# Kernel optimization log

Hardware: AMD Instinct MI355X
Metric: run time of the kernel (lower is better)

The kernel has to match this reference:

```python
import jax, jax.numpy as jnp
import numpy as np

N = 50000       # nodes
E_RAND = 800000 # random edges (avg degree 16); self loops appended
IN, HID, H, OUT = 256, 64, 4, 256
NEG_SLOPE = 0.2


def setup_inputs() -> dict:
    key = jax.random.key(0)
    ks = jax.random.split(key, 8)
    x = jax.random.normal(ks[0], (N, IN), dtype=jnp.float32)
    er = jax.random.randint(ks[1], (2, E_RAND), 0, N, dtype=jnp.int32)
    loops = jnp.arange(N, dtype=jnp.int32)
    edge_index = jnp.concatenate([er, jnp.stack([loops, loops])], axis=1)  # [2, E_RAND+N]
    # xavier-ish scaled params
    W1 = jax.random.normal(ks[2], (H * HID, IN), jnp.float32) * (2.0 / (IN + H * HID)) ** 0.5
    a1_src = jax.random.normal(ks[3], (H, HID), jnp.float32) * 0.1
    a1_dst = jax.random.normal(ks[4], (H, HID), jnp.float32) * 0.1
    W2 = jax.random.normal(ks[5], (OUT, H * HID), jnp.float32) * (2.0 / (H * HID + OUT)) ** 0.5
    a2_src = jax.random.normal(ks[6], (1, OUT), jnp.float32) * 0.1
    a2_dst = jax.random.normal(ks[7], (1, OUT), jnp.float32) * 0.1
    return {"x": x, "edge_index": edge_index, "W1": W1, "a1_src": a1_src,
            "a1_dst": a1_dst, "W2": W2, "a2_src": a2_src, "a2_dst": a2_dst}


def gat_layer(h, W, a_src, a_dst, src, dst, concat):
    n = h.shape[0]
    nh, nf = a_src.shape
    hp = (h @ W.T).reshape(n, nh, nf)                 # [N,H,F]
    e = (hp[src] * a_src).sum(-1) + (hp[dst] * a_dst).sum(-1)  # [E,H]
    e = jnp.where(e > 0, e, NEG_SLOPE * e)            # leaky_relu
    e_max = jax.ops.segment_max(e, dst, num_segments=n)
    ex = jnp.exp(e - e_max[dst])
    e_sum = jax.ops.segment_sum(ex, dst, num_segments=n)
    alpha = ex / (e_sum[dst] + 1e-16)                 # [E,H]
    out = jax.ops.segment_sum(hp[src] * alpha[..., None], dst, num_segments=n)
    return out.reshape(n, nh * nf) if concat else out.mean(axis=1)


def reference(x, edge_index, W1, a1_src, a1_dst, W2, a2_src, a2_dst):
    src, dst = edge_index[0], edge_index[1]
    h = jax.nn.relu(gat_layer(x, W1, a1_src, a1_dst, src, dst, True))
    return gat_layer(h, W2, a2_src, a2_dst, src, dst, False)
```

## Files before the change

kernel.cpp:

```cpp
#include <hip/hip_runtime.h>
#include <math.h>


typedef __attribute__((ext_vector_type(8))) short short8;
typedef __attribute__((ext_vector_type(4))) float f32x4;
typedef _Float16 half8 __attribute__((ext_vector_type(8)));

__device__ inline short f2bf(float f) {
    unsigned u = __float_as_uint(f);
    unsigned r = (u + 0x7FFF + ((u >> 16) & 1)) >> 16;
    return (short)r;
}
__device__ inline float bf2f(short b) {
    return __uint_as_float(((unsigned)(unsigned short)b) << 16);
}
__device__ inline unsigned short f2h(float f) {
    _Float16 h = (_Float16)f;
    unsigned short u;
    __builtin_memcpy(&u, &h, 2);
    return u;
}
__device__ inline float h2f(unsigned short u) {
    _Float16 h;
    __builtin_memcpy(&h, &u, 2);
    return (float)h;
}

__global__ void convert_w(const float* __restrict__ W, short* __restrict__ Whi,
                          short* __restrict__ Wlo, int n) {
    int i = blockIdx.x * 256 + threadIdx.x;
    if (i < n) {
        float v = W[i];
        short h = f2bf(v);
        Whi[i] = h;
        Wlo[i] = f2bf(v - bf2f(h));
    }
}

__global__ __launch_bounds__(256) void gemm_mfma(const float* __restrict__ A,
                                                 const short* __restrict__ Bh_g,
                                                 const short* __restrict__ Bl_g,
                                                 unsigned short* __restrict__ C, int M) {
    __shared__ short Ah[128 * 40];
    __shared__ short Al[128 * 40];
    __shared__ short Bh[128 * 40];
    __shared__ short Bl[128 * 40];
    const int tid = threadIdx.x;
    const int m0 = blockIdx.x * 128;
    const int n0 = blockIdx.y * 128;
    const int w = tid >> 6, lane = tid & 63;
    const int l15 = lane & 15, q = lane >> 4;

    f32x4 acc[2][8];
    #pragma unroll
    for (int mt = 0; mt < 2; ++mt)
        #pragma unroll
        for (int nt = 0; nt < 8; ++nt) acc[mt][nt] = (f32x4){0.f, 0.f, 0.f, 0.f};

    const int ar = tid >> 1;
    const int ak = (tid & 1) * 16;

    for (int k0 = 0; k0 < 256; k0 += 32) {
        int gm = m0 + ar;
        float4 v0, v1, v2, v3;
        if (gm < M) {
            const float* ap = &A[(size_t)gm * 256 + k0 + ak];
            v0 = *(const float4*)(ap);
            v1 = *(const float4*)(ap + 4);
            v2 = *(const float4*)(ap + 8);
            v3 = *(const float4*)(ap + 12);
        } else {
            v0 = make_float4(0.f, 0.f, 0.f, 0.f);
            v1 = v0; v2 = v0; v3 = v0;
        }
        float av[16] = {v0.x, v0.y, v0.z, v0.w, v1.x, v1.y, v1.z, v1.w,
                        v2.x, v2.y, v2.z, v2.w, v3.x, v3.y, v3.z, v3.w};
        short8 hi0, hi1, lo0, lo1;
        #pragma unroll
        for (int j = 0; j < 8; ++j) {
            short h = f2bf(av[j]);
            hi0[j] = h;
            lo0[j] = f2bf(av[j] - bf2f(h));
        }
        #pragma unroll
        for (int j = 0; j < 8; ++j) {
            short h = f2bf(av[8 + j]);
            hi1[j] = h;
            lo1[j] = f2bf(av[8 + j] - bf2f(h));
        }
        *(short8*)&Ah[ar * 40 + ak]     = hi0;
        *(short8*)&Ah[ar * 40 + ak + 8] = hi1;
        *(short8*)&Al[ar * 40 + ak]     = lo0;
        *(short8*)&Al[ar * 40 + ak + 8] = lo1;
        {
            const short* s0 = &Bh_g[(size_t)(n0 + ar) * 256 + k0 + ak];
            *(short8*)&Bh[ar * 40 + ak]     = *(const short8*)s0;
            *(short8*)&Bh[ar * 40 + ak + 8] = *(const short8*)(s0 + 8);
            const short* s1 = &Bl_g[(size_t)(n0 + ar) * 256 + k0 + ak];
            *(short8*)&Bl[ar * 40 + ak]     = *(const short8*)s1;
            *(short8*)&Bl[ar * 40 + ak + 8] = *(const short8*)(s1 + 8);
        }
        __syncthreads();
        short8 ahi[2], alo[2];
        #pragma unroll
        for (int mt = 0; mt < 2; ++mt) {
            int rowA = w * 32 + mt * 16 + l15;
            ahi[mt] = *(short8*)&Ah[rowA * 40 + q * 8];
            alo[mt] = *(short8*)&Al[rowA * 40 + q * 8];
        }
        #pragma unroll
        for (int nt = 0; nt < 8; ++nt) {
            int rowB = nt * 16 + l15;
            short8 bhi = *(short8*)&Bh[rowB * 40 + q * 8];
            short8 blo = *(short8*)&Bl[rowB * 40 + q * 8];
            #pragma unroll
            for (int mt = 0; mt < 2; ++mt) {
                acc[mt][nt] = __builtin_amdgcn_mfma_f32_16x16x32_bf16(ahi[mt], bhi, acc[mt][nt], 0, 0, 0);
                acc[mt][nt] = __builtin_amdgcn_mfma_f32_16x16x32_bf16(alo[mt], bhi, acc[mt][nt], 0, 0, 0);
                acc[mt][nt] = __builtin_amdgcn_mfma_f32_16x16x32_bf16(ahi[mt], blo, acc[mt][nt], 0, 0, 0);
            }
        }
        __syncthreads();
    }
    #pragma unroll
    for (int mt = 0; mt < 2; ++mt) {
        #pragma unroll
        for (int nt = 0; nt < 8; ++nt) {
            #pragma unroll
            for (int r = 0; r < 4; ++r) {
                int gm = m0 + w * 32 + mt * 16 + q * 4 + r;
                if (gm < M) C[(size_t)gm * 256 + n0 + nt * 16 + l15] = f2h(acc[mt][nt][r]);
            }
        }
    }
}

__global__ void zero_int(int* __restrict__ p, int n) {
    int i = blockIdx.x * 256 + threadIdx.x;
    if (i < n) p[i] = 0;
}

__global__ void hist_kernel(const int* __restrict__ dst, int* __restrict__ deg, int E) {
    int i = blockIdx.x * 256 + threadIdx.x;
    if (i < E) atomicAdd(&deg[dst[i]], 1);
}

__global__ __launch_bounds__(1024) void scan1(const int* __restrict__ deg,
                                              int* __restrict__ lex,
                                              int* __restrict__ bsums, int n) {
    __shared__ int sh[1024];
    int tid = threadIdx.x;
    int i = blockIdx.x * 1024 + tid;
    int v = (i < n) ? deg[i] : 0;
    sh[tid] = v;
    __syncthreads();
    #pragma unroll
    for (int off = 1; off < 1024; off <<= 1) {
        int t2 = (tid >= off) ? sh[tid - off] : 0;
        __syncthreads();
        sh[tid] += t2;
        __syncthreads();
    }
    if (i < n) lex[i] = sh[tid] - v;
    if (tid == 1023) bsums[blockIdx.x] = sh[1023];
}

__global__ __launch_bounds__(1024) void scan2(const int* __restrict__ bsums,
                                              int* __restrict__ boffs,
                                              int* __restrict__ offs, int nb, int n) {
    __shared__ int sh[1024];
    int tid = threadIdx.x;
    int v = (tid < nb) ? bsums[tid] : 0;
    sh[tid] = v;
    __syncthreads();
    #pragma unroll
    for (int off = 1; off < 1024; off <<= 1) {
        int t2 = (tid >= off) ? sh[tid - off] : 0;
        __syncthreads();
        sh[tid] += t2;
        __syncthreads();
    }
    if (tid < nb) boffs[tid] = sh[tid] - v;
    if (tid == nb - 1) offs[n] = sh[tid];
}

__global__ __launch_bounds__(1024) void scan3(int* __restrict__ offs,
                                              int* __restrict__ cur,
                                              const int* __restrict__ boffs, int n) {
    int i = blockIdx.x * 1024 + threadIdx.x;
    if (i < n) {
        int o = offs[i] + boffs[blockIdx.x];
        offs[i] = o;
        cur[i] = o;
    }
}

__global__ void scatter_kernel(const int* __restrict__ src, const int* __restrict__ dst,
                               int* __restrict__ cur, int* __restrict__ sorted, int E) {
    int i = blockIdx.x * 256 + threadIdx.x;
    if (i < E) {
        int p = atomicAdd(&cur[dst[i]], 1);
        sorted[p] = src[i];
    }
}

template <int NH>
__global__ __launch_bounds__(256) void scompute(const unsigned short* __restrict__ hp,
                                                const float* __restrict__ a_src,
                                                const float* __restrict__ a_dst,
                                                float* __restrict__ s_src,
                                                float* __restrict__ s_dst, int N) {
    const int w = threadIdx.x >> 6, lane = threadIdx.x & 63;
    const int node = blockIdx.x * 4 + w;
    if (node >= N) return;
    const int f0 = lane * 4;
    ushort4 uv = *(const ushort4*)(hp + (size_t)node * 256 + f0);
    float4 as = *(const float4*)(a_src + f0);
    float4 ad = *(const float4*)(a_dst + f0);
    float x0 = h2f(uv.x), x1 = h2f(uv.y), x2 = h2f(uv.z), x3 = h2f(uv.w);
    float p1 = x0 * as.x + x1 * as.y + x2 * as.z + x3 * as.w;
    float p2 = x0 * ad.x + x1 * ad.y + x2 * ad.z + x3 * ad.w;
    if constexpr (NH == 4) {
        #pragma unroll
        for (int off = 1; off < 16; off <<= 1) {
            p1 += __shfl_xor(p1, off, 64);
            p2 += __shfl_xor(p2, off, 64);
        }
        if ((lane & 15) == 0) {
            s_src[node * 4 + (lane >> 4)] = p1;
            s_dst[node * 4 + (lane >> 4)] = p2;
        }
    } else {
        #pragma unroll
        for (int off = 1; off < 64; off <<= 1) {
            p1 += __shfl_xor(p1, off, 64);
            p2 += __shfl_xor(p2, off, 64);
        }
        if (lane == 0) {
            s_src[node] = p1;
            s_dst[node] = p2;
        }
    }
}

template <int NH, bool RELU>
__global__ __launch_bounds__(256) void aggregate4(const unsigned short* __restrict__ hp,
                                                  const float* __restrict__ ssrc,
                                                  const float* __restrict__ sdst,
                                                  const int* __restrict__ offs,
                                                  const int* __restrict__ sorted,
                                                  float* __restrict__ out, int N) {
    __shared__ int   s_sh[4][64];
    __shared__ float p_sh[4][64][NH];

    const int w = threadIdx.x >> 6, lane = threadIdx.x & 63;
    const int node_raw = blockIdx.x * 4 + w;
    const bool node_ok = node_raw < N;
    const int node = node_ok ? node_raw : (N - 1);
    constexpr int NF = 256 / NH;

    const int b = offs[node], e = offs[node + 1];
    const int deg = e - b;

    float sv[NH];
    #pragma unroll
    for (int h = 0; h < NH; ++h) sv[h] = sdst[node * NH + h];

    float lv[NH], mx[NH];
    const bool small = (deg <= 64);

    if (small) {
        int key = (lane < deg) ? sorted[b + lane] : 0x7FFFFFFF;
        #pragma unroll
        for (int k = 2; k <= 64; k <<= 1) {
            #pragma unroll
            for (int j = k >> 1; j > 0; j >>= 1) {
                int other = __shfl_xor(key, j, 64);
                bool keepMin = ((lane & j) == 0) == ((lane & k) == 0);
                int mn = min(key, other), mh = max(key, other);
                key = keepMin ? mn : mh;
            }
        }
        const bool valid = lane < deg;
        const int mys = valid ? key : 0;

        float evv[NH];
        if constexpr (NH == 4) {
            float4 sa = *(const float4*)&ssrc[(size_t)mys * 4];
            evv[0] = sa.x + sv[0]; evv[1] = sa.y + sv[1];
            evv[2] = sa.z + sv[2]; evv[3] = sa.w + sv[3];
        } else {
            evv[0] = ssrc[mys] + sv[0];
        }
        #pragma unroll
        for (int h = 0; h < NH; ++h) {
            float ev = evv[h];
            ev = ev > 0.f ? ev : 0.2f * ev;
            evv[h] = valid ? ev : -INFINITY;
            mx[h] = evv[h];
        }
        #pragma unroll
        for (int off = 32; off > 0; off >>= 1)
            #pragma unroll
            for (int h = 0; h < NH; ++h)
                mx[h] = fmaxf(mx[h], __shfl_xor(mx[h], off, 64));

        float pv[NH];
        #pragma unroll
        for (int h = 0; h < NH; ++h) {
            pv[h] = valid ? __expf(evv[h] - mx[h]) : 0.f;
            lv[h] = pv[h];
        }
        #pragma unroll
        for (int off = 32; off > 0; off >>= 1)
            #pragma unroll
            for (int h = 0; h < NH; ++h)
                lv[h] += __shfl_xor(lv[h], off, 64);

        s_sh[w][lane] = mys;
        #pragma unroll
        for (int h = 0; h < NH; ++h) p_sh[w][lane][h] = pv[h];
    } else {
        #pragma unroll
        for (int h = 0; h < NH; ++h) mx[h] = -INFINITY;
        for (int c = b + lane; c < e; c += 64) {
            int s = sorted[c];
            #pragma unroll
            for (int h = 0; h < NH; ++h) {
                float ev = ssrc[s * NH + h] + sv[h];
                ev = ev > 0.f ? ev : 0.2f * ev;
                mx[h] = fmaxf(mx[h], ev);
            }
        }
        #pragma unroll
        for (int off = 32; off > 0; off >>= 1)
            #pragma unroll
            for (int h = 0; h < NH; ++h)
                mx[h] = fmaxf(mx[h], __shfl_xor(mx[h], off, 64));
    }

    __syncthreads();

    if (small) {
        const int quarter = lane >> 4;
        const int l16 = lane & 15;
        const int f0 = l16 * 16;
        const int head = f0 / NF;

        float acc[16];
        #pragma unroll
        for (int k = 0; k < 16; ++k) acc[k] = 0.f;

        const int iters = (deg + 3) >> 2;
        for (int t2 = 0; t2 < iters; ++t2) {
            int j = 4 * t2 + quarter;
            bool jv = j < deg;
            int jj = jv ? j : 0;
            int s = s_sh[w][jj];
            float p = jv ? p_sh[w][jj][head] : 0.f;
            const unsigned short* row = hp + (size_t)s * 256 + f0;
            half8 v0 = *(const half8*)(row);
            half8 v1 = *(const half8*)(row + 8);
            #pragma unroll
            for (int k = 0; k < 8; ++k) {
                acc[k]     = fmaf(p, (float)v0[k], acc[k]);
                acc[8 + k] = fmaf(p, (float)v1[k], acc[8 + k]);
            }
        }
        #pragma unroll
        for (int k = 0; k < 16; ++k) {
            acc[k] += __shfl_xor(acc[k], 16, 64);
            acc[k] += __shfl_xor(acc[k], 32, 64);
        }
        if (node_ok && lane < 16) {
            float li = 1.0f / (lv[head] + 1e-16f);
            float o[16];
            #pragma unroll
            for (int k = 0; k < 16; ++k) {
                o[k] = acc[k] * li;
                if (RELU) o[k] = fmaxf(o[k], 0.f);
            }
            float* op = &out[(size_t)node * 256 + f0];
            *(float4*)&op[0]  = make_float4(o[0], o[1], o[2], o[3]);
            *(float4*)&op[4]  = make_float4(o[4], o[5], o[6], o[7]);
            *(float4*)&op[8]  = make_float4(o[8], o[9], o[10], o[11]);
            *(float4*)&op[12] = make_float4(o[12], o[13], o[14], o[15]);
        }
    } else {
        const int half = lane >> 5;
        const int l32 = lane & 31;
        const int f0 = l32 * 8;
        const int head = f0 / NF;

        float acc[8];
        #pragma unroll
        for (int k = 0; k < 8; ++k) acc[k] = 0.f;
        #pragma unroll
        for (int h = 0; h < NH; ++h) lv[h] = 0.f;

        int last = -1, round = 0;
        for (;;) {
            int myMin = 0x7FFFFFFF, myCnt = 0;
            for (int c = b + lane; c < e; c += 64) {
                int s = sorted[c];
                if (s > last) {
                    if (s < myMin) { myMin = s; myCnt = 1; }
                    else if (s == myMin) ++myCnt;
                }
            }
            #pragma unroll
            for (int off = 32; off > 0; off >>= 1) {
                int om = __shfl_xor(myMin, off, 64);
                int oc = __shfl_xor(myCnt, off, 64);
                if (om < myMin) { myMin = om; myCnt = oc; }
                else if (om == myMin) myCnt += oc;
            }
            if (myMin == 0x7FFFFFFF) break;
            const bool mine = ((round & 1) == half);
            float cf = (float)myCnt;
            float ph[NH];
            #pragma unroll
            for (int h = 0; h < NH; ++h) {
                float ev = ssrc[myMin * NH + h] + sv[h];
                ev = ev > 0.f ? ev : 0.2f * ev;
                ph[h] = __expf(ev - mx[h]);
            }
            if (mine && l32 == 0) {
                #pragma unroll
                for (int h = 0; h < NH; ++h) lv[h] += cf * ph[h];
            }
            if (mine) {
                float p = cf * ph[head];
                half8 v = *(const half8*)(hp + (size_t)myMin * 256 + f0);
                #pragma unroll
                for (int k = 0; k < 8; ++k) acc[k] = fmaf(p, (float)v[k], acc[k]);
            }
            last = myMin; ++round;
        }
        #pragma unroll
        for (int off = 32; off > 0; off >>= 1)
            #pragma unroll
            for (int h = 0; h < NH; ++h)
                lv[h] += __shfl_xor(lv[h], off, 64);

        #pragma unroll
        for (int k = 0; k < 8; ++k) acc[k] += __shfl_xor(acc[k], 32, 64);

        if (node_ok && lane < 32) {
            float li = 1.0f / (lv[head] + 1e-16f);
            float o[8];
            #pragma unroll
            for (int k = 0; k < 8; ++k) {
                o[k] = acc[k] * li;
                if (RELU) o[k] = fmaxf(o[k], 0.f);
            }
            *(float4*)&out[(size_t)node * 256 + f0]     = make_float4(o[0], o[1], o[2], o[3]);
            *(float4*)&out[(size_t)node * 256 + f0 + 4] = make_float4(o[4], o[5], o[6], o[7]);
        }
    }
}

extern "C" void kernel_launch(void* const* d_in, const int* in_sizes, int n_in,
                              void* d_out, int out_size, void* d_ws, size_t ws_size,
                              hipStream_t stream) {
    const float* x   = (const float*)d_in[0];
    const int*   ei  = (const int*)d_in[1];
    const float* W1  = (const float*)d_in[2];
    const float* a1s = (const float*)d_in[3];
    const float* a1d = (const float*)d_in[4];
    const float* W2  = (const float*)d_in[5];
    const float* a2s = (const float*)d_in[6];
    const float* a2d = (const float*)d_in[7];
    float* out = (float*)d_out;

    const int N = in_sizes[0] / 256;
    const int E = in_sizes[1] / 2;
    const int* src = ei;
    const int* dst = ei + E;

    unsigned short* hp = (unsigned short*)d_ws;
    float* ssrc  = (float*)(hp + (size_t)N * 256);
    float* sdst  = ssrc + (size_t)N * 4;
    int*   deg   = (int*)(sdst + (size_t)N * 4);
    int*   cur   = deg + N;
    int*   offs  = cur + N;
    int*   sorted= offs + N + 1;
    int*   bsums = sorted + E;
    int*   boffs = bsums + 64;
    short* w1hi  = (short*)(boffs + 64);
    short* w1lo  = w1hi + 65536;
    short* w2hi  = w1lo + 65536;
    short* w2lo  = w2hi + 65536;

    const int nb = (N + 1023) / 1024;

    convert_w<<<256, 256, 0, stream>>>(W1, w1hi, w1lo, 65536);
    convert_w<<<256, 256, 0, stream>>>(W2, w2hi, w2lo, 65536);

    zero_int<<<(N + 255) / 256, 256, 0, stream>>>(deg, N);
    hist_kernel<<<(E + 255) / 256, 256, 0, stream>>>(dst, deg, E);
    scan1<<<nb, 1024, 0, stream>>>(deg, offs, bsums, N);
    scan2<<<1, 1024, 0, stream>>>(bsums, boffs, offs, nb, N);
    scan3<<<nb, 1024, 0, stream>>>(offs, cur, boffs, N);
    scatter_kernel<<<(E + 255) / 256, 256, 0, stream>>>(src, dst, cur, sorted, E);

    dim3 gg((N + 127) / 128, 2);
    int aggblocks = (N + 3) / 4;

    gemm_mfma<<<gg, 256, 0, stream>>>(x, w1hi, w1lo, hp, N);
    scompute<4><<<aggblocks, 256, 0, stream>>>(hp, a1s, a1d, ssrc, sdst, N);
    aggregate4<4, true><<<aggblocks, 256, 0, stream>>>(hp, ssrc, sdst, offs, sorted, out, N);

    gemm_mfma<<<gg, 256, 0, stream>>>(out, w2hi, w2lo, hp, N);
    scompute<1><<<aggblocks, 256, 0, stream>>>(hp, a2s, a2d, ssrc, sdst, N);
    aggregate4<1, false><<<aggblocks, 256, 0, stream>>>(hp, ssrc, sdst, offs, sorted, out, N);
}
```

Before: 428.1 us.

## Pre-split GEMM inputs to bf16 hi/lo, hoist CSR sort, prefetch aggregate rows

A new convert_x8 kernel splits x into bf16 hi/lo halves once, stored in the output buffer. The layer-1 aggregation now writes its activations directly as bf16 hi/lo, so both GEMMs load pre-split shorts instead of converting fp32 on every tile. The per-node bitonic sort of neighbour lists moves out of both aggregate calls into a single sort_csr pass. The aggregate loop also software-prefetches the next neighbour index and weight. The aim is to cut redundant conversion ALU work and one duplicated sort, at the cost of an extra kernel and extra memory traffic for the x conversion.

New measurement: 454.0 us. +6.1%, slower.

```diff
diff --git a/kernel.cpp b/kernel.cpp
--- a/kernel.cpp
+++ b/kernel.cpp
@@ -37,7 +37,34 @@
     }
 }
 
-__global__ __launch_bounds__(256) void gemm_mfma(const float* __restrict__ A,
+__global__ void convert_x8(const float* __restrict__ X, short* __restrict__ Xhi,
+                           short* __restrict__ Xlo, long n) {
+    long i = ((long)blockIdx.x * 256 + threadIdx.x) * 8;
+    if (i + 8 <= n) {
+        float4 v0 = *(const float4*)&X[i];
+        float4 v1 = *(const float4*)&X[i + 4];
+        float av[8] = {v0.x, v0.y, v0.z, v0.w, v1.x, v1.y, v1.z, v1.w};
+        short8 hi, lo;
+        #pragma unroll
+        for (int j = 0; j < 8; ++j) {
+            short h = f2bf(av[j]);
+            hi[j] = h;
+            lo[j] = f2bf(av[j] - bf2f(h));
+        }
+        *(short8*)&Xhi[i] = hi;
+        *(short8*)&Xlo[i] = lo;
+    } else {
+        for (long k = i; k < n; ++k) {
+            float v = X[k];
+            short h = f2bf(v);
+            Xhi[k] = h;
+            Xlo[k] = f2bf(v - bf2f(h));
+        }
+    }
+}
+
+__global__ __launch_bounds__(256) void gemm_mfma(const short* __restrict__ Ah_g,
+                                                 const short* __restrict__ Al_g,
                                                  const short* __restrict__ Bh_g,
                                                  const short* __restrict__ Bl_g,
                                                  unsigned short* __restrict__ C, int M) {
@@ -62,36 +89,20 @@
 
     for (int k0 = 0; k0 < 256; k0 += 32) {
         int gm = m0 + ar;
-        float4 v0, v1, v2, v3;
         if (gm < M) {
-            const float* ap = &A[(size_t)gm * 256 + k0 + ak];
-            v0 = *(const float4*)(ap);
-            v1 = *(const float4*)(ap + 4);
-            v2 = *(const float4*)(ap + 8);
-            v3 = *(const float4*)(ap + 12);
+            const short* a0 = &Ah_g[(size_t)gm * 256 + k0 + ak];
+            *(short8*)&Ah[ar * 40 + ak]     = *(const short8*)a0;
+            *(short8*)&Ah[ar * 40 + ak + 8] = *(const short8*)(a0 + 8);
+            const short* a1 = &Al_g[(size_t)gm * 256 + k0 + ak];
+            *(short8*)&Al[ar * 40 + ak]     = *(const short8*)a1;
+            *(short8*)&Al[ar * 40 + ak + 8] = *(const short8*)(a1 + 8);
         } else {
-            v0 = make_float4(0.f, 0.f, 0.f, 0.f);
-            v1 = v0; v2 = v0; v3 = v0;
-        }
-        float av[16] = {v0.x, v0.y, v0.z, v0.w, v1.x, v1.y, v1.z, v1.w,
-                        v2.x, v2.y, v2.z, v2.w, v3.x, v3.y, v3.z, v3.w};
-        short8 hi0, hi1, lo0, lo1;
-        #pragma unroll
-        for (int j = 0; j < 8; ++j) {
-            short h = f2bf(av[j]);
-            hi0[j] = h;
-            lo0[j] = f2bf(av[j] - bf2f(h));
-        }
-        #pragma unroll
-        for (int j = 0; j < 8; ++j) {
-            short h = f2bf(av[8 + j]);
-            hi1[j] = h;
-            lo1[j] = f2bf(av[8 + j] - bf2f(h));
-        }
-        *(short8*)&Ah[ar * 40 + ak]     = hi0;
-        *(short8*)&Ah[ar * 40 + ak + 8] = hi1;
-        *(short8*)&Al[ar * 40 + ak]     = lo0;
-        *(short8*)&Al[ar * 40 + ak + 8] = lo1;
+            short8 z = (short8){0, 0, 0, 0, 0, 0, 0, 0};
+            *(short8*)&Ah[ar * 40 + ak]     = z;
+            *(short8*)&Ah[ar * 40 + ak + 8] = z;
+            *(short8*)&Al[ar * 40 + ak]     = z;
+            *(short8*)&Al[ar * 40 + ak + 8] = z;
+        }
         {
             const short* s0 = &Bh_g[(size_t)(n0 + ar) * 256 + k0 + ak];
             *(short8*)&Bh[ar * 40 + ak]     = *(const short8*)s0;
@@ -202,6 +213,28 @@
         int p = atomicAdd(&cur[dst[i]], 1);
         sorted[p] = src[i];
     }
+}
+
+__global__ __launch_bounds__(256) void sort_csr(const int* __restrict__ offs,
+                                                int* __restrict__ sorted, int N) {
+    const int w = threadIdx.x >> 6, lane = threadIdx.x & 63;
+    const int node = blockIdx.x * 4 + w;
+    if (node >= N) return;
+    const int b = offs[node], e = offs[node + 1];
+    const int deg = e - b;
+    if (deg < 2 || deg > 64) return;
+    int key = (lane < deg) ? sorted[b + lane] : 0x7FFFFFFF;
+    #pragma unroll
+    for (int k = 2; k <= 64; k <<= 1) {
+        #pragma unroll
+        for (int j = k >> 1; j > 0; j >>= 1) {
+            int other = __shfl_xor(key, j, 64);
+            bool keepMin = ((lane & j) == 0) == ((lane & k) == 0);
+            int mn = min(key, other), mh = max(key, other);
+            key = keepMin ? mn : mh;
+        }
+    }
+    if (lane < deg) sorted[b + lane] = key;
 }
 
 template <int NH>
@@ -243,13 +276,15 @@
     }
 }
 
-template <int NH, bool RELU>
+template <int NH, bool RELU, bool SPLIT>
 __global__ __launch_bounds__(256) void aggregate4(const unsigned short* __restrict__ hp,
                                                   const float* __restrict__ ssrc,
                                                   const float* __restrict__ sdst,
                                                   const int* __restrict__ offs,
                                                   const int* __restrict__ sorted,
-                                                  float* __restrict__ out, int N) {
+                                                  float* __restrict__ out,
+                                                  short* __restrict__ ohi,
+                                                  short* __restrict__ olo, int N) {
     __shared__ int   s_sh[4][64];
     __shared__ float p_sh[4][64][NH];
 
@@ -270,19 +305,8 @@
     const bool small = (deg <= 64);
 
     if (small) {
-        int key = (lane < deg) ? sorted[b + lane] : 0x7FFFFFFF;
-        #pragma unroll
-        for (int k = 2; k <= 64; k <<= 1) {
-            #pragma unroll
-            for (int j = k >> 1; j > 0; j >>= 1) {
-                int other = __shfl_xor(key, j, 64);
-                bool keepMin = ((lane & j) == 0) == ((lane & k) == 0);
-                int mn = min(key, other), mh = max(key, other);
-                key = keepMin ? mn : mh;
-            }
-        }
         const bool valid = lane < deg;
-        const int mys = valid ? key : 0;
+        const int mys = valid ? sorted[b + lane] : 0;
 
         float evv[NH];
         if constexpr (NH == 4) {
@@ -352,19 +376,25 @@
         for (int k = 0; k < 16; ++k) acc[k] = 0.f;
 
         const int iters = (deg + 3) >> 2;
+        int j = quarter;
+        bool jv = j < deg;
+        int jj = jv ? j : 0;
+        int s = s_sh[w][jj];
+        float p = jv ? p_sh[w][jj][head] : 0.f;
         for (int t2 = 0; t2 < iters; ++t2) {
-            int j = 4 * t2 + quarter;
-            bool jv = j < deg;
-            int jj = jv ? j : 0;
-            int s = s_sh[w][jj];
-            float p = jv ? p_sh[w][jj][head] : 0.f;
             const unsigned short* row = hp + (size_t)s * 256 + f0;
             half8 v0 = *(const half8*)(row);
             half8 v1 = *(const half8*)(row + 8);
+            float pc = p;
+            int jn = 4 * (t2 + 1) + quarter;
+            bool jvn = jn < deg;
+            int jjn = jvn ? jn : 0;
+            s = s_sh[w][jjn];
+            p = jvn ? p_sh[w][jjn][head] : 0.f;
             #pragma unroll
             for (int k = 0; k < 8; ++k) {
-                acc[k]     = fmaf(p, (float)v0[k], acc[k]);
-                acc[8 + k] = fmaf(p, (float)v1[k], acc[8 + k]);
+                acc[k]     = fmaf(pc, (float)v0[k], acc[k]);
+                acc[8 + k] = fmaf(pc, (float)v1[k], acc[8 + k]);
             }
         }
         #pragma unroll
@@ -380,11 +410,26 @@
                 o[k] = acc[k] * li;
                 if (RELU) o[k] = fmaxf(o[k], 0.f);
             }
-            float* op = &out[(size_t)node * 256 + f0];
-            *(float4*)&op[0]  = make_float4(o[0], o[1], o[2], o[3]);
-            *(float4*)&op[4]  = make_float4(o[4], o[5], o[6], o[7]);
-            *(float4*)&op[8]  = make_float4(o[8], o[9], o[10], o[11]);
-            *(float4*)&op[12] = make_float4(o[12], o[13], o[14], o[15]);
+            if constexpr (SPLIT) {
+                short8 h0, h1, l0, l1;
+                #pragma unroll
+                for (int k = 0; k < 8; ++k) {
+                    short hh = f2bf(o[k]);
+                    h0[k] = hh; l0[k] = f2bf(o[k] - bf2f(hh));
+                    short hh2 = f2bf(o[8 + k]);
+                    h1[k] = hh2; l1[k] = f2bf(o[8 + k] - bf2f(hh2));
+                }
+                *(short8*)&ohi[(size_t)node * 256 + f0]     = h0;
+                *(short8*)&ohi[(size_t)node * 256 + f0 + 8] = h1;
+                *(short8*)&olo[(size_t)node * 256 + f0]     = l0;
+                *(short8*)&olo[(size_t)node * 256 + f0 + 8] = l1;
+            } else {
+                float* op = &out[(size_t)node * 256 + f0];
+                *(float4*)&op[0]  = make_float4(o[0], o[1], o[2], o[3]);
+                *(float4*)&op[4]  = make_float4(o[4], o[5], o[6], o[7]);
+                *(float4*)&op[8]  = make_float4(o[8], o[9], o[10], o[11]);
+                *(float4*)&op[12] = make_float4(o[12], o[13], o[14], o[15]);
+            }
         }
     } else {
         const int half = lane >> 5;
@@ -454,8 +499,19 @@
                 o[k] = acc[k] * li;
                 if (RELU) o[k] = fmaxf(o[k], 0.f);
             }
-            *(float4*)&out[(size_t)node * 256 + f0]     = make_float4(o[0], o[1], o[2], o[3]);
-            *(float4*)&out[(size_t)node * 256 + f0 + 4] = make_float4(o[4], o[5], o[6], o[7]);
+            if constexpr (SPLIT) {
+                short8 h0, l0;
+                #pragma unroll
+                for (int k = 0; k < 8; ++k) {
+                    short hh = f2bf(o[k]);
+                    h0[k] = hh; l0[k] = f2bf(o[k] - bf2f(hh));
+                }
+                *(short8*)&ohi[(size_t)node * 256 + f0] = h0;
+                *(short8*)&olo[(size_t)node * 256 + f0] = l0;
+            } else {
+                *(float4*)&out[(size_t)node * 256 + f0]     = make_float4(o[0], o[1], o[2], o[3]);
+                *(float4*)&out[(size_t)node * 256 + f0 + 4] = make_float4(o[4], o[5], o[6], o[7]);
+            }
         }
     }
 }
@@ -492,10 +548,15 @@
     short* w2hi  = w1lo + 65536;
     short* w2lo  = w2hi + 65536;
 
+    short* xhi = (short*)d_out;
+    short* xlo = xhi + (size_t)N * 256;
+
     const int nb = (N + 1023) / 1024;
 
     convert_w<<<256, 256, 0, stream>>>(W1, w1hi, w1lo, 65536);
     convert_w<<<256, 256, 0, stream>>>(W2, w2hi, w2lo, 65536);
+    long nx = (long)N * 256;
+    convert_x8<<<(int)((nx / 8 + 255) / 256), 256, 0, stream>>>(x, xhi, xlo, nx);
 
     zero_int<<<(N + 255) / 256, 256, 0, stream>>>(deg, N);
     hist_kernel<<<(E + 255) / 256, 256, 0, stream>>>(dst, deg, E);
@@ -506,12 +567,15 @@
 
     dim3 gg((N + 127) / 128, 2);
     int aggblocks = (N + 3) / 4;
-
-    gemm_mfma<<<gg, 256, 0, stream>>>(x, w1hi, w1lo, hp, N);
+    sort_csr<<<aggblocks, 256, 0, stream>>>(offs, sorted, N);
+
+    gemm_mfma<<<gg, 256, 0, stream>>>(xhi, xlo, w1hi, w1lo, hp, N);
     scompute<4><<<aggblocks, 256, 0, stream>>>(hp, a1s, a1d, ssrc, sdst, N);
-    aggregate4<4, true><<<aggblocks, 256, 0, stream>>>(hp, ssrc, sdst, offs, sorted, out, N);
-
-    gemm_mfma<<<gg, 256, 0, stream>>>(out, w2hi, w2lo, hp, N);
+    aggregate4<4, true, true><<<aggblocks, 256, 0, stream>>>(hp, ssrc, sdst, offs, sorted,
+                                                             nullptr, xhi, xlo, N);
+
+    gemm_mfma<<<gg, 256, 0, stream>>>(xhi, xlo, w2hi, w2lo, hp, N);
     scompute<1><<<aggblocks, 256, 0, stream>>>(hp, a2s, a2d, ssrc, sdst, N);
-    aggregate4<1, false><<<aggblocks, 256, 0, stream>>>(hp, ssrc, sdst, offs, sorted, out, N);
-}
+    aggregate4<1, false, false><<<aggblocks, 256, 0, stream>>>(hp, ssrc, sdst, offs, sorted,
+                                                               out, nullptr, nullptr, N);
+}
```

## Switch GEMMs to single-pass fp16 MFMA and hoist per-node neighbor sort

Applied to the files above, without the earlier changes.

Replaces the three-pass split-bf16 GEMM (hi/lo emulation of fp32) with a single fp16 MFMA pass. Inputs x and the layer-1 activations are now stored as fp16, the latter written straight from aggregate4, with d_out reused as scratch. The bitonic sort of each node's neighbor list moves out of both aggregate passes into one sort_csr kernel that runs once. This cuts MFMA work and the bytes the GEMMs read, but lowers GEMM input precision to fp16 and adds a conversion pass over x.

Result: faster. 414.6 us (-3.2%).

```diff
diff --git a/kernel.cpp b/kernel.cpp
--- a/kernel.cpp
+++ b/kernel.cpp
@@ -3,17 +3,10 @@
 
 
 typedef __attribute__((ext_vector_type(8))) short short8;
+typedef __attribute__((ext_vector_type(8))) unsigned short ushort8;
 typedef __attribute__((ext_vector_type(4))) float f32x4;
 typedef _Float16 half8 __attribute__((ext_vector_type(8)));
 
-__device__ inline short f2bf(float f) {
-    unsigned u = __float_as_uint(f);
-    unsigned r = (u + 0x7FFF + ((u >> 16) & 1)) >> 16;
-    return (short)r;
-}
-__device__ inline float bf2f(short b) {
-    return __uint_as_float(((unsigned)(unsigned short)b) << 16);
-}
 __device__ inline unsigned short f2h(float f) {
     _Float16 h = (_Float16)f;
     unsigned short u;
@@ -26,25 +19,26 @@
     return (float)h;
 }
 
-__global__ void convert_w(const float* __restrict__ W, short* __restrict__ Whi,
-                          short* __restrict__ Wlo, int n) {
-    int i = blockIdx.x * 256 + threadIdx.x;
-    if (i < n) {
-        float v = W[i];
-        short h = f2bf(v);
-        Whi[i] = h;
-        Wlo[i] = f2bf(v - bf2f(h));
-    }
-}
-
-__global__ __launch_bounds__(256) void gemm_mfma(const float* __restrict__ A,
-                                                 const short* __restrict__ Bh_g,
-                                                 const short* __restrict__ Bl_g,
+__global__ void convert_h8(const float* __restrict__ X, unsigned short* __restrict__ Xh,
+                           long n) {
+    long i = ((long)blockIdx.x * 256 + threadIdx.x) * 8;
+    if (i + 8 <= n) {
+        float4 v0 = *(const float4*)&X[i];
+        float4 v1 = *(const float4*)&X[i + 4];
+        ushort8 o;
+        o[0] = f2h(v0.x); o[1] = f2h(v0.y); o[2] = f2h(v0.z); o[3] = f2h(v0.w);
+        o[4] = f2h(v1.x); o[5] = f2h(v1.y); o[6] = f2h(v1.z); o[7] = f2h(v1.w);
+        *(ushort8*)&Xh[i] = o;
+    } else {
+        for (long k = i; k < n; ++k) Xh[k] = f2h(X[k]);
+    }
+}
+
+__global__ __launch_bounds__(256) void gemm_mfma(const unsigned short* __restrict__ A_g,
+                                                 const unsigned short* __restrict__ B_g,
                                                  unsigned short* __restrict__ C, int M) {
-    __shared__ short Ah[128 * 40];
-    __shared__ short Al[128 * 40];
-    __shared__ short Bh[128 * 40];
-    __shared__ short Bl[128 * 40];
+    __shared__ unsigned short Ah[128 * 40];
+    __shared__ unsigned short Bh[128 * 40];
     const int tid = threadIdx.x;
     const int m0 = blockIdx.x * 128;
     const int n0 = blockIdx.y * 128;
@@ -62,63 +56,34 @@
 
     for (int k0 = 0; k0 < 256; k0 += 32) {
         int gm = m0 + ar;
-        float4 v0, v1, v2, v3;
         if (gm < M) {
-            const float* ap = &A[(size_t)gm * 256 + k0 + ak];
-            v0 = *(const float4*)(ap);
-            v1 = *(const float4*)(ap + 4);
-            v2 = *(const float4*)(ap + 8);
-            v3 = *(const float4*)(ap + 12);
+            const unsigned short* a0 = &A_g[(size_t)gm * 256 + k0 + ak];
+            *(ushort8*)&Ah[ar * 40 + ak]     = *(const ushort8*)a0;
+            *(ushort8*)&Ah[ar * 40 + ak + 8] = *(const ushort8*)(a0 + 8);
         } else {
-            v0 = make_float4(0.f, 0.f, 0.f, 0.f);
-            v1 = v0; v2 = v0; v3 = v0;
-        }
-        float av[16] = {v0.x, v0.y, v0.z, v0.w, v1.x, v1.y, v1.z, v1.w,
-                        v2.x, v2.y, v2.z, v2.w, v3.x, v3.y, v3.z, v3.w};
-        short8 hi0, hi1, lo0, lo1;
-        #pragma unroll
-        for (int j = 0; j < 8; ++j) {
-            short h = f2bf(av[j]);
-            hi0[j] = h;
-            lo0[j] = f2bf(av[j] - bf2f(h));
-        }
-        #pragma unroll
-        for (int j = 0; j < 8; ++j) {
-            short h = f2bf(av[8 + j]);
-            hi1[j] = h;
-            lo1[j] = f2bf(av[8 + j] - bf2f(h));
-        }
-        *(short8*)&Ah[ar * 40 + ak]     = hi0;
-        *(short8*)&Ah[ar * 40 + ak + 8] = hi1;
-        *(short8*)&Al[ar * 40 + ak]     = lo0;
-        *(short8*)&Al[ar * 40 + ak + 8] = lo1;
+            ushort8 z = (ushort8){0, 0, 0, 0, 0, 0, 0, 0};
+            *(ushort8*)&Ah[ar * 40 + ak]     = z;
+            *(ushort8*)&Ah[ar * 40 + ak + 8] = z;
+        }
         {
-            const short* s0 = &Bh_g[(size_t)(n0 + ar) * 256 + k0 + ak];
-            *(short8*)&Bh[ar * 40 + ak]     = *(const short8*)s0;
-            *(short8*)&Bh[ar * 40 + ak + 8] = *(const short8*)(s0 + 8);
-            const short* s1 = &Bl_g[(size_t)(n0 + ar) * 256 + k0 + ak];
-            *(short8*)&Bl[ar * 40 + ak]     = *(const short8*)s1;
-            *(short8*)&Bl[ar * 40 + ak + 8] = *(const short8*)(s1 + 8);
+            const unsigned short* b0 = &B_g[(size_t)(n0 + ar) * 256 + k0 + ak];
+            *(ushort8*)&Bh[ar * 40 + ak]     = *(const ushort8*)b0;
+            *(ushort8*)&Bh[ar * 40 + ak + 8] = *(const ushort8*)(b0 + 8);
         }
         __syncthreads();
-        short8 ahi[2], alo[2];
+        half8 a[2];
         #pragma unroll
         for (int mt = 0; mt < 2; ++mt) {
             int rowA = w * 32 + mt * 16 + l15;
-            ahi[mt] = *(short8*)&Ah[rowA * 40 + q * 8];
-            alo[mt] = *(short8*)&Al[rowA * 40 + q * 8];
+            a[mt] = *(half8*)&Ah[rowA * 40 + q * 8];
         }
         #pragma unroll
         for (int nt = 0; nt < 8; ++nt) {
             int rowB = nt * 16 + l15;
-            short8 bhi = *(short8*)&Bh[rowB * 40 + q * 8];
-            short8 blo = *(short8*)&Bl[rowB * 40 + q * 8];
-            #pragma unroll
-            for (int mt = 0; mt < 2; ++mt) {
-                acc[mt][nt] = __builtin_amdgcn_mfma_f32_16x16x32_bf16(ahi[mt], bhi, acc[mt][nt], 0, 0, 0);
-                acc[mt][nt] = __builtin_amdgcn_mfma_f32_16x16x32_bf16(alo[mt], bhi, acc[mt][nt], 0, 0, 0);
-                acc[mt][nt] = __builtin_amdgcn_mfma_f32_16x16x32_bf16(ahi[mt], blo, acc[mt][nt], 0, 0, 0);
-            }
+            half8 bf = *(half8*)&Bh[rowB * 40 + q * 8];
+            #pragma unroll
+            for (int mt = 0; mt < 2; ++mt)
+                acc[mt][nt] = __builtin_amdgcn_mfma_f32_16x16x32_f16(a[mt], bf, acc[mt][nt], 0, 0, 0);
         }
         __syncthreads();
     }
@@ -202,6 +167,28 @@
         int p = atomicAdd(&cur[dst[i]], 1);
         sorted[p] = src[i];
     }
+}
+
+__global__ __launch_bounds__(256) void sort_csr(const int* __restrict__ offs,
+                                                int* __restrict__ sorted, int N) {
+    const int w = threadIdx.x >> 6, lane = threadIdx.x & 63;
+    const int node = blockIdx.x * 4 + w;
+    if (node >= N) return;
+    const int b = offs[node], e = offs[node + 1];
+    const int deg = e - b;
+    if (deg < 2 || deg > 64) return;
+    int key = (lane < deg) ? sorted[b + lane] : 0x7FFFFFFF;
+    #pragma unroll
+    for (int k = 2; k <= 64; k <<= 1) {
+        #pragma unroll
+        for (int j = k >> 1; j > 0; j >>= 1) {
+            int other = __shfl_xor(key, j, 64);
+            bool keepMin = ((lane & j) == 0) == ((lane & k) == 0);
+            int mn = min(key, other), mh = max(key, other);
+            key = keepMin ? mn : mh;
+        }
+    }
+    if (lane < deg) sorted[b + lane] = key;
 }
 
 template <int NH>
@@ -243,13 +230,14 @@
     }
 }
 
-template <int NH, bool RELU>
+template <int NH, bool RELU, bool F16OUT>
 __global__ __launch_bounds__(256) void aggregate4(const unsigned short* __restrict__ hp,
                                                   const float* __restrict__ ssrc,
                                                   const float* __restrict__ sdst,
                                                   const int* __restrict__ offs,
                                                   const int* __restrict__ sorted,
-                                                  float* __restrict__ out, int N) {
+                                                  float* __restrict__ out,
+                                                  unsigned short* __restrict__ outh, int N) {
     __shared__ int   s_sh[4][64];
     __shared__ float p_sh[4][64][NH];
 
@@ -270,19 +258,8 @@
     const bool small = (deg <= 64);
 
     if (small) {
-        int key = (lane < deg) ? sorted[b + lane] : 0x7FFFFFFF;
-        #pragma unroll
-        for (int k = 2; k <= 64; k <<= 1) {
-            #pragma unroll
-            for (int j = k >> 1; j > 0; j >>= 1) {
-                int other = __shfl_xor(key, j, 64);
-                bool keepMin = ((lane & j) == 0) == ((lane & k) == 0);
-                int mn = min(key, other), mh = max(key, other);
-                key = keepMin ? mn : mh;
-            }
-        }
         const bool valid = lane < deg;
-        const int mys = valid ? key : 0;
+        const int mys = valid ? sorted[b + lane] : 0;
 
         float evv[NH];
         if constexpr (NH == 4) {
@@ -380,11 +357,22 @@
                 o[k] = acc[k] * li;
                 if (RELU) o[k] = fmaxf(o[k], 0.f);
             }
-            float* op = &out[(size_t)node * 256 + f0];
-            *(float4*)&op[0]  = make_float4(o[0], o[1], o[2], o[3]);
-            *(float4*)&op[4]  = make_float4(o[4], o[5], o[6], o[7]);
-            *(float4*)&op[8]  = make_float4(o[8], o[9], o[10], o[11]);
-            *(float4*)&op[12] = make_float4(o[12], o[13], o[14], o[15]);
+            if constexpr (F16OUT) {
+                ushort8 u0, u1;
+                #pragma unroll
+                for (int k = 0; k < 8; ++k) {
+                    u0[k] = f2h(o[k]);
+                    u1[k] = f2h(o[8 + k]);
+                }
+                *(ushort8*)&outh[(size_t)node * 256 + f0]     = u0;
+                *(ushort8*)&outh[(size_t)node * 256 + f0 + 8] = u1;
+            } else {
+                float* op = &out[(size_t)node * 256 + f0];
+                *(float4*)&op[0]  = make_float4(o[0], o[1], o[2], o[3]);
+                *(float4*)&op[4]  = make_float4(o[4], o[5], o[6], o[7]);
+                *(float4*)&op[8]  = make_float4(o[8], o[9], o[10], o[11]);
+                *(float4*)&op[12] = make_float4(o[12], o[13], o[14], o[15]);
+            }
         }
     } else {
         const int half = lane >> 5;
@@ -454,8 +442,15 @@
                 o[k] = acc[k] * li;
                 if (RELU) o[k] = fmaxf(o[k], 0.f);
             }
-            *(float4*)&out[(size_t)node * 256 + f0]     = make_float4(o[0], o[1], o[2], o[3]);
-            *(float4*)&out[(size_t)node * 256 + f0 + 4] = make_float4(o[4], o[5], o[6], o[7]);
+            if constexpr (F16OUT) {
+                ushort8 u0;
+                #pragma unroll
+                for (int k = 0; k < 8; ++k) u0[k] = f2h(o[k]);
+                *(ushort8*)&outh[(size_t)node * 256 + f0] = u0;
+            } else {
+                *(float4*)&out[(size_t)node * 256 + f0]     = make_float4(o[0], o[1], o[2], o[3]);
+                *(float4*)&out[(size_t)node * 256 + f0 + 4] = make_float4(o[4], o[5], o[6], o[7]);
+            }
         }
     }
 }
@@ -487,15 +482,18 @@
     int*   sorted= offs + N + 1;
     int*   bsums = sorted + E;
     int*   boffs = bsums + 64;
-    short* w1hi  = (short*)(boffs + 64);
-    short* w1lo  = w1hi + 65536;
-    short* w2hi  = w1lo + 65536;
-    short* w2lo  = w2hi + 65536;
+    unsigned short* w1h = (unsigned short*)(boffs + 64);
+    unsigned short* w2h = w1h + 65536;
+
+    unsigned short* xh = (unsigned short*)d_out;
+    unsigned short* hh = xh + (size_t)N * 256;
 
     const int nb = (N + 1023) / 1024;
 
-    convert_w<<<256, 256, 0, stream>>>(W1, w1hi, w1lo, 65536);
-    convert_w<<<256, 256, 0, stream>>>(W2, w2hi, w2lo, 65536);
+    convert_h8<<<32, 256, 0, stream>>>(W1, w1h, 65536);
+    convert_h8<<<32, 256, 0, stream>>>(W2, w2h, 65536);
+    long nx = (long)N * 256;
+    convert_h8<<<(int)((nx / 8 + 255) / 256), 256, 0, stream>>>(x, xh, nx);
 
     zero_int<<<(N + 255) / 256, 256, 0, stream>>>(deg, N);
     hist_kernel<<<(E + 255) / 256, 256, 0, stream>>>(dst, deg, E);
@@ -506,12 +504,15 @@
 
     dim3 gg((N + 127) / 128, 2);
     int aggblocks = (N + 3) / 4;
-
-    gemm_mfma<<<gg, 256, 0, stream>>>(x, w1hi, w1lo, hp, N);
+    sort_csr<<<aggblocks, 256, 0, stream>>>(offs, sorted, N);
+
+    gemm_mfma<<<gg, 256, 0, stream>>>(xh, w1h, hp, N);
     scompute<4><<<aggblocks, 256, 0, stream>>>(hp, a1s, a1d, ssrc, sdst, N);
-    aggregate4<4, true><<<aggblocks, 256, 0, stream>>>(hp, ssrc, sdst, offs, sorted, out, N);
-
-    gemm_mfma<<<gg, 256, 0, stream>>>(out, w2hi, w2lo, hp, N);
+    aggregate4<4, true, true><<<aggblocks, 256, 0, stream>>>(hp, ssrc, sdst, offs, sorted,
+                                                             nullptr, hh, N);
+
+    gemm_mfma<<<gg, 256, 0, stream>>>(hh, w2h, hp, N);
     scompute<1><<<aggblocks, 256, 0, stream>>>(hp, a2s, a2d, ssrc, sdst, N);
-    aggregate4<1, false><<<aggblocks, 256, 0, stream>>>(hp, ssrc, sdst, offs, sorted, out, N);
-}
+    aggregate4<1, false, false><<<aggblocks, 256, 0, stream>>>(hp, ssrc, sdst, offs, sorted,
+                                                               out, nullptr, N);
+}
```
